# Kernel tuning notes

Hardware: AMD Instinct MI355X
Metric: run time of the kernel (lower is better)

Reference implementation:

```python
import jax, jax.numpy as jnp
import numpy as np

B, S, E = 2, 4096, 640
H, D, G = 4, 256, 1      # n_heads, head_dim, n_kv_groups
WINDOW = 512
SCALING = 256.0 ** -0.5  # query_pre_attn_scalar ** -0.5
EPS = 1e-6


def rmsnorm(x, scale):
    # Gemma variant: weight = 1 + scale, computed in fp32 over last dim
    xf = x.astype(jnp.float32)
    var = jnp.mean(xf * xf, axis=-1, keepdims=True)
    return (xf * jax.lax.rsqrt(var + EPS) * (1.0 + scale.astype(jnp.float32))).astype(x.dtype)


def apply_rope(x, cos, sin):
    # x: [B, h, S, D]; cos/sin: [S, D]
    half = x.shape[-1] // 2
    x1, x2 = x[..., :half], x[..., half:]
    rotated = jnp.concatenate([-x2, x1], axis=-1)
    return (x * cos[None, None] + rotated * sin[None, None]).astype(x.dtype)


def setup_inputs() -> dict:
    key = jax.random.key(0)
    ks = jax.random.split(key, 6)
    x = jax.random.normal(ks[0], (B, S, E), dtype=jnp.float32)
    # weights (torch Linear weight.T layout: [in, out])
    Wq = jax.random.normal(ks[1], (E, H * D), dtype=jnp.float32) * 0.02
    Wk = jax.random.normal(ks[2], (E, G * D), dtype=jnp.float32) * 0.02
    Wv = jax.random.normal(ks[3], (E, G * D), dtype=jnp.float32) * 0.02
    Wo = jax.random.normal(ks[4], (H * D, E), dtype=jnp.float32) * 0.02
    q_scale = jnp.zeros((D,), dtype=jnp.float32)
    k_scale = jnp.zeros((D,), dtype=jnp.float32)
    # RoPE tables (theta = rope_local_base = 10000 for sliding layers)
    inv_freq = 1.0 / (10000.0 ** (jnp.arange(0, D, 2, dtype=jnp.float32) / D))
    angles = jnp.arange(S, dtype=jnp.float32)[:, None] * inv_freq[None, :]
    angles = jnp.concatenate([angles, angles], axis=1)  # [S, D]
    cos, sin = jnp.cos(angles), jnp.sin(angles)
    # causal + sliding-window mask; True = masked out
    i = jnp.arange(S)[:, None]
    j = jnp.arange(S)[None, :]
    mask = (j > i) | ((i - j) >= WINDOW)
    return {"x": x, "mask": mask, "cos": cos, "sin": sin,
            "Wq": Wq, "Wk": Wk, "Wv": Wv, "Wo": Wo,
            "q_scale": q_scale, "k_scale": k_scale}


def reference(x, mask, cos, sin, Wq, Wk, Wv, Wo, q_scale, k_scale):
    b, s, _ = x.shape
    q = (x @ Wq).reshape(b, s, H, D).transpose(0, 2, 1, 3)  # [B,H,S,D]
    k = (x @ Wk).reshape(b, s, G, D).transpose(0, 2, 1, 3)  # [B,G,S,D]
    v = (x @ Wv).reshape(b, s, G, D).transpose(0, 2, 1, 3)  # [B,G,S,D]
    q = rmsnorm(q, q_scale)
    k = rmsnorm(k, k_scale)
    q = apply_rope(q, cos, sin)
    k = apply_rope(k, cos, sin)
    # GQA: K/V have G=1 heads; broadcasting replaces repeat_interleave
    scores = (q * SCALING) @ jnp.swapaxes(k, -1, -2)  # [B,H,S,S]
    scores = jnp.where(mask[None, None], -jnp.inf, scores)
    attn = jax.nn.softmax(scores, axis=-1)
    out = attn @ v                                     # [B,H,S,D]
    out = out.transpose(0, 2, 1, 3).reshape(b, s, H * D)
    return out @ Wo
```

## Files before the change

### kernel.cpp

```cpp
#include <hip/hip_runtime.h>
#include <hip/hip_bf16.h>
#include <stdint.h>

#define BB 2
#define SS 4096
#define EE 640
#define HH 4
#define DD 256
#define WIN 512

typedef __attribute__((ext_vector_type(8))) short bv8;
typedef __attribute__((ext_vector_type(4))) float fv4;
typedef __attribute__((ext_vector_type(16))) float fv16;

__device__ __forceinline__ unsigned short f2b(float f) {
  union { float f; unsigned u; } a; a.f = f;
  unsigned r = a.u + 0x7fffu + ((a.u >> 16) & 1u);
  return (unsigned short)(r >> 16);
}
__device__ __forceinline__ float b2f(unsigned short s) {
  union { unsigned u; float f; } a; a.u = ((unsigned)s) << 16;
  return a.f;
}
__device__ __forceinline__ unsigned pk2(float lo, float hi_) {
  return (unsigned)f2b(lo) | ((unsigned)f2b(hi_) << 16);
}

typedef const __attribute__((address_space(1))) unsigned int* as1u;
typedef __attribute__((address_space(3))) unsigned int* as3u;
__device__ __forceinline__ void gld16(const unsigned short* g, unsigned short* l) {
  __builtin_amdgcn_global_load_lds((as1u)(const void*)g, (as3u)(void*)l, 16, 0, 0);
}

__global__ __launch_bounds__(256) void k_cast_bf16(const float* __restrict__ src,
                                                   unsigned short* __restrict__ dst, int n4) {
  int i = blockIdx.x * 256 + threadIdx.x;
  if (i >= n4) return;
  fv4 v = ((const fv4*)src)[i];
  ushort4 o; o.x = f2b(v.x); o.y = f2b(v.y); o.z = f2b(v.z); o.w = f2b(v.w);
  ((ushort4*)dst)[i] = o;
}

__global__ __launch_bounds__(256) void k_wtrans(const float* __restrict__ Wq,
    const float* __restrict__ Wk, const float* __restrict__ Wv,
    const float* __restrict__ Wo, unsigned short* __restrict__ wqkv,
    unsigned short* __restrict__ wo) {
  __shared__ float tile[32][33];
  const int z = blockIdx.z, bx = blockIdx.x, by = blockIdx.y;
  const float* src; unsigned short* dst; int ss, ds;
  if (z == 0)      { if (bx >= 20 || by >= 32) return; src = Wq; dst = wqkv;              ss = 1024; ds = 640; }
  else if (z == 1) { if (bx >= 20 || by >= 8)  return; src = Wk; dst = wqkv + 1024 * 640; ss = 256;  ds = 640; }
  else if (z == 2) { if (bx >= 20 || by >= 8)  return; src = Wv; dst = wqkv + 1280 * 640; ss = 256;  ds = 640; }
  else             { if (bx >= 32 || by >= 20) return; src = Wo; dst = wo;                ss = 640;  ds = 1024; }
  int r0 = bx * 32, c0 = by * 32;
  int t = threadIdx.x;
  int rr = t >> 3, cc = (t & 7) * 4;
  fv4 x = *(const fv4*)(src + (size_t)(r0 + rr) * ss + c0 + cc);
#pragma unroll
  for (int i = 0; i < 4; ++i) tile[cc + i][rr] = x[i];
  __syncthreads();
  ushort4 o;
  o.x = f2b(tile[rr][cc + 0]); o.y = f2b(tile[rr][cc + 1]);
  o.z = f2b(tile[rr][cc + 2]); o.w = f2b(tile[rr][cc + 3]);
  *(ushort4*)(dst + (size_t)(c0 + rr) * ds + r0 + cc) = o;
}

__global__ __launch_bounds__(256) void k_vtrans(const unsigned short* __restrict__ qkv,
    unsigned short* __restrict__ vt) {
  __shared__ float tile[32][33];
  const int z = blockIdx.z;
  const unsigned short* src = qkv + (size_t)z * 4096 * 1536 + 1280;
  unsigned short* dst = vt + (size_t)z * 256 * 4096;
  int r0 = blockIdx.x * 32, c0 = blockIdx.y * 32;
  int t = threadIdx.x;
  int rr = t >> 3, cc = (t & 7) * 4;
  ushort4 x = *(const ushort4*)(src + (size_t)(r0 + rr) * 1536 + c0 + cc);
  tile[cc + 0][rr] = b2f(x.x); tile[cc + 1][rr] = b2f(x.y);
  tile[cc + 2][rr] = b2f(x.z); tile[cc + 3][rr] = b2f(x.w);
  __syncthreads();
  ushort4 o;
  o.x = f2b(tile[rr][cc + 0]); o.y = f2b(tile[rr][cc + 1]);
  o.z = f2b(tile[rr][cc + 2]); o.w = f2b(tile[rr][cc + 3]);
  *(ushort4*)(dst + (size_t)(c0 + rr) * 4096 + r0 + cc) = o;
}

template <bool OUT_BF16, int BN>
__global__ __launch_bounds__(256) void k_gemm(const unsigned short* __restrict__ A,
    const unsigned short* __restrict__ Bt, void* __restrict__ Cp,
    int M, int N, int K, int nt_n) {
  __shared__ unsigned short la[2][128 * 32];
  __shared__ unsigned short lb[2][BN * 32];
  const int bid = blockIdx.x;
  const int gidx = (bid & 7) * (gridDim.x >> 3) + (bid >> 3);
  const int m0 = (gidx / nt_n) * 128, n0 = (gidx % nt_n) * BN;
  const int tid = threadIdx.x, lane = tid & 63, wave = tid >> 6;
  const int g = lane >> 4, lr = lane & 15;
  constexpr int MI = (BN == 128) ? 4 : 2;
  const int wm = (BN == 128) ? (wave >> 1) * 64 : wave * 32;
  const int wn = (BN == 128) ? (wave & 1) * 64 : 0;
  fv4 acc[MI][4] = {};
  const int srow = wave * 32 + (lane >> 2);
  const int sch = (lane & 3) * 8;
  const unsigned short* ga0 = A + (size_t)(m0 + srow) * K + sch;
  const int srowb = (BN == 128) ? srow : (wave * 16 + (lane >> 2));
  const unsigned short* gb0 = Bt + (size_t)(n0 + srowb) * K + sch;
  const int NIT = K >> 5;
  auto stage = [&](int k0, int pp) {
    unsigned short* lad = la[pp] + wave * 1024;
    unsigned short* lbd = lb[pp] + ((BN == 128) ? wave * 1024 : wave * 512);
    gld16(ga0 + k0, lad);
    gld16(ga0 + (size_t)16 * K + k0, lad + 512);
    gld16(gb0 + k0, lbd);
    if constexpr (BN == 128) gld16(gb0 + (size_t)16 * K + k0, lbd + 512);
  };
  stage(0, 0);
  for (int it = 0; it < NIT; ++it) {
    const int p = it & 1;
    if (it > 0) __builtin_amdgcn_s_barrier();
    if (it + 1 < NIT) {
      stage((it + 1) * 32, p ^ 1);
      if constexpr (BN == 128)
        asm volatile("s_waitcnt vmcnt(4)" ::: "memory");
      else
        asm volatile("s_waitcnt vmcnt(3)" ::: "memory");
    } else {
      asm volatile("s_waitcnt vmcnt(0)" ::: "memory");
    }
    __builtin_amdgcn_sched_barrier(0);
    __builtin_amdgcn_s_barrier();
    bv8 af[MI], bf[4];
#pragma unroll
    for (int mi = 0; mi < MI; ++mi)
      af[mi] = *(const bv8*)(la[p] + (wm + mi * 16 + lr) * 32 + g * 8);
#pragma unroll
    for (int ni = 0; ni < 4; ++ni)
      bf[ni] = *(const bv8*)(lb[p] + (wn + ni * 16 + lr) * 32 + g * 8);
    __builtin_amdgcn_s_setprio(1);
#pragma unroll
    for (int mi = 0; mi < MI; ++mi)
#pragma unroll
      for (int ni = 0; ni < 4; ++ni)
        acc[mi][ni] = __builtin_amdgcn_mfma_f32_16x16x32_bf16(af[mi], bf[ni], acc[mi][ni], 0, 0, 0);
    __builtin_amdgcn_s_setprio(0);
  }
#pragma unroll
  for (int mi = 0; mi < MI; ++mi) {
#pragma unroll
    for (int r = 0; r < 4; ++r) {
      size_t row = (size_t)(m0 + wm + mi * 16 + g * 4 + r);
#pragma unroll
      for (int ni = 0; ni < 4; ++ni) {
        int col = n0 + wn + ni * 16 + lr;
        float val = acc[mi][ni][r];
        if constexpr (OUT_BF16)
          ((unsigned short*)Cp)[row * N + col] = f2b(val);
        else
          ((float*)Cp)[row * N + col] = val;
      }
    }
  }
}

__global__ __launch_bounds__(320) void k_normrope(const unsigned short* __restrict__ qkv,
    const float* __restrict__ cosp, const float* __restrict__ sinp,
    const float* __restrict__ qsc, const float* __restrict__ ksc,
    unsigned short* __restrict__ qo, unsigned short* __restrict__ ko) {
  int m = blockIdx.x;
  int b = m >> 12, s = m & 4095;
  int wave = threadIdx.x >> 6, lane = threadIdx.x & 63;
  bool isq = wave < 4;
  const unsigned short* src = qkv + (size_t)m * 1536 + (isq ? wave * 256 : 1024);
  const float* scp = isq ? qsc : ksc;
  int d0 = lane * 4;
  ushort4 raw = *(const ushort4*)(src + d0);
  float x0 = b2f(raw.x), x1 = b2f(raw.y), x2 = b2f(raw.z), x3 = b2f(raw.w);
  float ss = x0 * x0 + x1 * x1 + x2 * x2 + x3 * x3;
#pragma unroll
  for (int off = 1; off < 64; off <<= 1) ss += __shfl_xor(ss, off, 64);
  float rs = rsqrtf(ss * (1.0f / 256.0f) + 1e-6f);
  fv4 sc = *(const fv4*)(scp + d0);
  float n0 = x0 * rs * (1.0f + sc.x);
  float n1 = x1 * rs * (1.0f + sc.y);
  float n2 = x2 * rs * (1.0f + sc.z);
  float n3 = x3 * rs * (1.0f + sc.w);
  float p0 = __shfl_xor(n0, 32, 64);
  float p1 = __shfl_xor(n1, 32, 64);
  float p2 = __shfl_xor(n2, 32, 64);
  float p3 = __shfl_xor(n3, 32, 64);
  float sgn = (lane < 32) ? -1.0f : 1.0f;
  fv4 c4 = *(const fv4*)(cosp + (size_t)s * 256 + d0);
  fv4 s4 = *(const fv4*)(sinp + (size_t)s * 256 + d0);
  float mult = isq ? (0.0625f * 1.44269504f) : 1.0f;
  float o0 = (n0 * c4.x + sgn * p0 * s4.x) * mult;
  float o1 = (n1 * c4.y + sgn * p1 * s4.y) * mult;
  float o2 = (n2 * c4.z + sgn * p2 * s4.z) * mult;
  float o3 = (n3 * c4.w + sgn * p3 * s4.w) * mult;
  ushort4 o; o.x = f2b(o0); o.y = f2b(o1); o.z = f2b(o2); o.w = f2b(o3);
  unsigned short* dst = isq
      ? qo + ((size_t)(b * HH + wave) * SS + s) * 256 + d0
      : ko + ((size_t)b * SS + s) * 256 + d0;
  *(ushort4*)dst = o;
}

__global__ __launch_bounds__(512, 2) void k_attn(const unsigned short* __restrict__ q,
    const unsigned short* __restrict__ kg, const unsigned short* __restrict__ vtg,
    unsigned short* __restrict__ att) {
  __shared__ __align__(16) char ldsbuf[133120];
  __shared__ float lsb[4][32];
  unsigned short* kt = (unsigned short*)ldsbuf;
  unsigned short* vl = (unsigned short*)ldsbuf + 32768;
  const int bid = blockIdx.x;
  const int gidx = (bid & 7) * 32 + (bid >> 3);
  const int b = gidx >> 7;
  const int i0 = (gidx & 127) * 32;
  const int tid = threadIdx.x, wave = tid >> 6, lane = tid & 63;
  const int h = wave >> 1, ks = wave & 1;
  const int hi = lane >> 5, l31 = lane & 31;
  bv8 qf[16];
  {
    const unsigned short* qp = q + ((size_t)(b * HH + h) * SS + i0 + l31) * 256;
#pragma unroll
    for (int m = 0; m < 16; ++m) qf[m] = *(const bv8*)(qp + m * 16 + hi * 8);
  }
  fv16 po[8] = {};
  float lsp = 0.f;
  const int t0 = (i0 >= WIN) ? ((i0 - WIN + 1) >> 6) : 0;
  const int t1 = i0 >> 6;
  const unsigned short* kb = kg + (size_t)b * SS * 256;
  const unsigned short* vb = vtg + (size_t)b * 256 * SS;
  auto stageK = [&](int t, int pp) {
    const unsigned short* kbase = kb + (size_t)t * 64 * 256;
    unsigned short* dst = kt + pp * 16384;
#pragma unroll
    for (int c = 0; c < 4; ++c) {
      int slot = c * 512 + tid;
      int row = slot >> 5, s = slot & 31;
      gld16(kbase + (size_t)row * 256 + ((s ^ (row & 7)) * 8),
            dst + (c * 512 + wave * 64) * 8);
    }
  };
  auto stageV = [&](int t, int pp) {
    const unsigned short* vbase = vb + (size_t)t * 64;
    unsigned short* dst = vl + pp * 16384;
#pragma unroll
    for (int c = 0; c < 4; ++c) {
      int slot = c * 512 + tid;
      int d_ = slot >> 3, s = slot & 7;
      gld16(vbase + (size_t)d_ * SS + ((s ^ (d_ & 7)) * 8),
            dst + (c * 512 + wave * 64) * 8);
    }
  };
  stageK(t0, 0); stageV(t0, 0);
  int p = 0;
  const int krow = ks * 32 + l31;
  const int krx = krow & 7;
  const int vrx = l31 & 7;
  const float FSUB = 16.5f * 1.44269504f;
  for (int t = t0; t <= t1; ++t) {
    __syncthreads();
    if (t < t1) { stageK(t + 1, p ^ 1); stageV(t + 1, p ^ 1); }
    fv16 sa = {};
    const unsigned short* ktp = kt + p * 16384 + krow * 256;
    __builtin_amdgcn_s_setprio(1);
#pragma unroll
    for (int m = 0; m < 16; ++m) {
      bv8 kf = *(const bv8*)(ktp + (((m * 2 + hi) ^ krx) * 8));
      sa = __builtin_amdgcn_mfma_f32_32x32x16_bf16(kf, qf[m], sa, 0, 0, 0);
    }
    __builtin_amdgcn_s_setprio(0);
    const int kb0 = t * 64 + ks * 32;
    const bool nm = (kb0 + 31 > i0) || (i0 + 31 - kb0 >= WIN);
    if (nm) {
      const int qa = i0 + l31;
#pragma unroll
      for (int r = 0; r < 16; ++r) {
        int j = kb0 + (r & 3) + 8 * (r >> 2) + 4 * hi;
        if (j > qa || qa - j >= WIN) sa[r] = -1e30f;
      }
    }
    unsigned a[8];
#pragma unroll
    for (int i = 0; i < 8; ++i) {
      float e0 = exp2f(sa[2 * i] - FSUB);
      float e1 = exp2f(sa[2 * i + 1] - FSUB);
      lsp += e0 + e1;
      a[i] = pk2(e0, e1);
    }
    const unsigned short* vlp = vl + p * 16384;
    __builtin_amdgcn_s_setprio(1);
#pragma unroll
    for (int m2 = 0; m2 < 2; ++m2) {
      auto r02 = __builtin_amdgcn_permlane32_swap(a[m2 * 4 + 0], a[m2 * 4 + 2], false, false);
      auto r13 = __builtin_amdgcn_permlane32_swap(a[m2 * 4 + 1], a[m2 * 4 + 3], false, false);
      union { unsigned u[4]; bv8 v; } pf;
      pf.u[0] = r02[0]; pf.u[1] = r13[0]; pf.u[2] = r02[1]; pf.u[3] = r13[1];
      const int slot = (ks * 4 + m2 * 2 + hi) ^ vrx;
#pragma unroll
      for (int ds_ = 0; ds_ < 8; ++ds_) {
        bv8 vf = *(const bv8*)(vlp + (ds_ * 32 + l31) * 64 + slot * 8);
        po[ds_] = __builtin_amdgcn_mfma_f32_32x32x16_bf16(vf, pf.v, po[ds_], 0, 0, 0);
      }
    }
    __builtin_amdgcn_s_setprio(0);
    p ^= 1;
  }
  float lsfull = lsp + __shfl_xor(lsp, 32, 64);
  __syncthreads();
  float* cb = (float*)ldsbuf;
  if (ks == 1) {
#pragma unroll
    for (int ds_ = 0; ds_ < 8; ++ds_)
#pragma unroll
      for (int j = 0; j < 4; ++j) {
        int d0 = ds_ * 32 + 8 * j + 4 * hi;
        fv4 v4; v4[0] = po[ds_][4 * j]; v4[1] = po[ds_][4 * j + 1];
        v4[2] = po[ds_][4 * j + 2]; v4[3] = po[ds_][4 * j + 3];
        *(fv4*)(cb + (h * 32 + l31) * 260 + d0) = v4;
      }
    if (lane < 32) lsb[h][lane] = lsfull;
  }
  __syncthreads();
  if (ks == 0) {
    float total = lsfull + lsb[h][l31];
    float inv = 1.0f / total;
    unsigned short* op = att + ((size_t)b * SS + i0 + l31) * 1024 + h * 256;
#pragma unroll
    for (int ds_ = 0; ds_ < 8; ++ds_)
#pragma unroll
      for (int j = 0; j < 4; ++j) {
        int d0 = ds_ * 32 + 8 * j + 4 * hi;
        fv4 v4 = *(const fv4*)(cb + (h * 32 + l31) * 260 + d0);
        ushort4 o;
        o.x = f2b((po[ds_][4 * j] + v4[0]) * inv);
        o.y = f2b((po[ds_][4 * j + 1] + v4[1]) * inv);
        o.z = f2b((po[ds_][4 * j + 2] + v4[2]) * inv);
        o.w = f2b((po[ds_][4 * j + 3] + v4[3]) * inv);
        *(ushort4*)(op + d0) = o;
      }
  }
}

extern "C" void kernel_launch(void* const* d_in, const int* in_sizes, int n_in,
                              void* d_out, int out_size, void* d_ws, size_t ws_size,
                              hipStream_t stream) {
  const float* x    = (const float*)d_in[0];
  const float* cosp = (const float*)d_in[2];
  const float* sinp = (const float*)d_in[3];
  const float* Wq   = (const float*)d_in[4];
  const float* Wk   = (const float*)d_in[5];
  const float* Wv   = (const float*)d_in[6];
  const float* Wo   = (const float*)d_in[7];
  const float* qsc  = (const float*)d_in[8];
  const float* ksc  = (const float*)d_in[9];
  float* out = (float*)d_out;
  char* ws = (char*)d_ws;

  unsigned short* xb   = (unsigned short*)(ws);
  unsigned short* wqkv = (unsigned short*)(ws + 10485760);
  unsigned short* wo   = (unsigned short*)(ws + 12451840);
  unsigned short* qkv  = (unsigned short*)(ws + 13762560);
  unsigned short* qb   = (unsigned short*)(ws + 38928384);
  unsigned short* kbuf = (unsigned short*)(ws + 55705600);
  unsigned short* vt   = (unsigned short*)(ws + 59899904);
  unsigned short* attb = (unsigned short*)(ws + 64094208);

  k_cast_bf16<<<5120, 256, 0, stream>>>(x, xb, 1310720);
  k_wtrans<<<dim3(32, 32, 4), 256, 0, stream>>>(Wq, Wk, Wv, Wo, wqkv, wo);
  k_gemm<true, 128><<<768, 256, 0, stream>>>(xb, wqkv, qkv, 8192, 1536, 640, 12);
  k_normrope<<<8192, 320, 0, stream>>>(qkv, cosp, sinp, qsc, ksc, qb, kbuf);
  k_vtrans<<<dim3(128, 8, 2), 256, 0, stream>>>(qkv, vt);
  k_attn<<<256, 512, 0, stream>>>(qb, kbuf, vt, attb);
  k_gemm<false, 64><<<640, 256, 0, stream>>>(attb, wo, out, 8192, 640, 1024, 10);
}
```

Before: 115.0 us.

## Fuse QKV projection with RMSNorm, RoPE and V transpose epilogue

Replaces the separate QKV GEMM, norm+rope kernel and V-transpose kernel with one GEMM whose tiles are 64x256, so each N-tile covers exactly one head. The epilogue stages the tile in shared memory and applies RMSNorm and RoPE for Q/K heads, or writes V transposed directly. This removes the round trip of the bf16 qkv intermediate through global memory and two kernel launches. In exchange the GEMM tile shape changes (smaller M, larger shared footprint, more registers), which may reduce GEMM efficiency.

```diff
diff --git a/kernel.cpp b/kernel.cpp
--- a/kernel.cpp
+++ b/kernel.cpp
@@ -65,23 +65,142 @@
   *(ushort4*)(dst + (size_t)(c0 + rr) * ds + r0 + cc) = o;
 }
 
-__global__ __launch_bounds__(256) void k_vtrans(const unsigned short* __restrict__ qkv,
+__global__ __launch_bounds__(256) void k_gemm_qkv(const unsigned short* __restrict__ A,
+    const unsigned short* __restrict__ Bt,
+    const float* __restrict__ cosp, const float* __restrict__ sinp,
+    const float* __restrict__ qsc, const float* __restrict__ ksc,
+    unsigned short* __restrict__ qo, unsigned short* __restrict__ ko,
     unsigned short* __restrict__ vt) {
-  __shared__ float tile[32][33];
-  const int z = blockIdx.z;
-  const unsigned short* src = qkv + (size_t)z * 4096 * 1536 + 1280;
-  unsigned short* dst = vt + (size_t)z * 256 * 4096;
-  int r0 = blockIdx.x * 32, c0 = blockIdx.y * 32;
-  int t = threadIdx.x;
-  int rr = t >> 3, cc = (t & 7) * 4;
-  ushort4 x = *(const ushort4*)(src + (size_t)(r0 + rr) * 1536 + c0 + cc);
-  tile[cc + 0][rr] = b2f(x.x); tile[cc + 1][rr] = b2f(x.y);
-  tile[cc + 2][rr] = b2f(x.z); tile[cc + 3][rr] = b2f(x.w);
+  __shared__ __align__(16) char shl[40960];
+  unsigned short* la = (unsigned short*)shl;
+  unsigned short* lb = (unsigned short*)(shl + 8192);
+  const int K = EE;
+  const int bid = blockIdx.x;
+  const int gidx = (bid & 7) * 96 + (bid >> 3);
+  const int mt = gidx / 6, nt = gidx % 6;
+  const int m0 = mt * 64, n0 = nt * 256;
+  const int tid = threadIdx.x, lane = tid & 63, wave = tid >> 6;
+  const int g = lane >> 4, lr = lane & 15;
+  const int wm = (wave >> 1) * 32, wn = (wave & 1) * 128;
+  fv4 acc[2][8] = {};
+  const unsigned short* ga0 = A + (size_t)(m0 + (tid >> 2)) * K + (tid & 3) * 8;
+  const unsigned short* gb0 = Bt + (size_t)(n0 + (tid >> 2)) * K + (tid & 3) * 8;
+  auto stage = [&](int k0, int pp) {
+    gld16(ga0 + k0, la + pp * 2048 + wave * 512);
+#pragma unroll
+    for (int c = 0; c < 4; ++c)
+      gld16(gb0 + (size_t)(c * 64) * K + k0, lb + pp * 8192 + (c * 64 + wave * 16) * 32);
+  };
+  stage(0, 0);
+  const int NIT = K >> 5;
+  for (int it = 0; it < NIT; ++it) {
+    const int p = it & 1;
+    if (it > 0) __builtin_amdgcn_s_barrier();
+    if (it + 1 < NIT) {
+      stage((it + 1) * 32, p ^ 1);
+      asm volatile("s_waitcnt vmcnt(5)" ::: "memory");
+    } else {
+      asm volatile("s_waitcnt vmcnt(0)" ::: "memory");
+    }
+    __builtin_amdgcn_sched_barrier(0);
+    __builtin_amdgcn_s_barrier();
+    bv8 af[2], bf[8];
+#pragma unroll
+    for (int mi = 0; mi < 2; ++mi)
+      af[mi] = *(const bv8*)(la + p * 2048 + (wm + mi * 16 + lr) * 32 + g * 8);
+#pragma unroll
+    for (int ni = 0; ni < 8; ++ni)
+      bf[ni] = *(const bv8*)(lb + p * 8192 + (wn + ni * 16 + lr) * 32 + g * 8);
+    __builtin_amdgcn_s_setprio(1);
+#pragma unroll
+    for (int mi = 0; mi < 2; ++mi)
+#pragma unroll
+      for (int ni = 0; ni < 8; ++ni)
+        acc[mi][ni] = __builtin_amdgcn_mfma_f32_16x16x32_bf16(af[mi], bf[ni], acc[mi][ni], 0, 0, 0);
+    __builtin_amdgcn_s_setprio(0);
+  }
   __syncthreads();
-  ushort4 o;
-  o.x = f2b(tile[rr][cc + 0]); o.y = f2b(tile[rr][cc + 1]);
-  o.z = f2b(tile[rr][cc + 2]); o.w = f2b(tile[rr][cc + 3]);
-  *(ushort4*)(dst + (size_t)(c0 + rr) * 4096 + r0 + cc) = o;
+  unsigned short* cw = (unsigned short*)shl;
+  float* rsum = (float*)(shl + 33792);
+#pragma unroll
+  for (int mi = 0; mi < 2; ++mi)
+#pragma unroll
+    for (int r = 0; r < 4; ++r) {
+      int row = wm + mi * 16 + g * 4 + r;
+#pragma unroll
+      for (int ni = 0; ni < 8; ++ni)
+        cw[row * 264 + wn + ni * 16 + lr] = f2b(acc[mi][ni][r]);
+    }
+  __syncthreads();
+  const int m = m0 + (tid & 63);
+  const int b = m >> 12, s = m & 4095;
+  if (nt < 5) {
+    const int qq = tid >> 6;
+    const int row = tid & 63;
+    const int dlo = qq * 32, dhi = dlo + 128;
+    float xlo[32], xhi[32];
+    float ss2 = 0.f;
+#pragma unroll
+    for (int j8 = 0; j8 < 4; ++j8) {
+      bv8 v0 = *(const bv8*)(cw + row * 264 + dlo + j8 * 8);
+      bv8 v1 = *(const bv8*)(cw + row * 264 + dhi + j8 * 8);
+#pragma unroll
+      for (int e = 0; e < 8; ++e) {
+        float a0 = b2f((unsigned short)v0[e]);
+        float a1 = b2f((unsigned short)v1[e]);
+        xlo[j8 * 8 + e] = a0; xhi[j8 * 8 + e] = a1;
+        ss2 += a0 * a0 + a1 * a1;
+      }
+    }
+    rsum[row * 4 + qq] = ss2;
+    __syncthreads();
+    float tot = rsum[row * 4 + 0] + rsum[row * 4 + 1] + rsum[row * 4 + 2] + rsum[row * 4 + 3];
+    float rs = rsqrtf(tot * (1.0f / 256.0f) + 1e-6f);
+    const float* scp = (nt < 4) ? qsc : ksc;
+    const float mult = (nt < 4) ? (0.0625f * 1.44269504f) : 1.0f;
+    unsigned short* dst = (nt < 4)
+        ? qo + ((size_t)(b * HH + nt) * SS + s) * 256
+        : ko + ((size_t)b * SS + s) * 256;
+    const float* crow = cosp + (size_t)s * 256;
+    const float* srow = sinp + (size_t)s * 256;
+#pragma unroll
+    for (int j4 = 0; j4 < 8; ++j4) {
+      fv4 sclo = *(const fv4*)(scp + dlo + j4 * 4);
+      fv4 schi = *(const fv4*)(scp + dhi + j4 * 4);
+      fv4 clo = *(const fv4*)(crow + dlo + j4 * 4);
+      fv4 chi = *(const fv4*)(crow + dhi + j4 * 4);
+      fv4 slo = *(const fv4*)(srow + dlo + j4 * 4);
+      fv4 shi = *(const fv4*)(srow + dhi + j4 * 4);
+      ushort4 olo, ohi;
+#pragma unroll
+      for (int e = 0; e < 4; ++e) {
+        float nlo = xlo[j4 * 4 + e] * rs * (1.0f + sclo[e]);
+        float nhi = xhi[j4 * 4 + e] * rs * (1.0f + schi[e]);
+        float rlo = (nlo * clo[e] - nhi * slo[e]) * mult;
+        float rhi = (nhi * chi[e] + nlo * shi[e]) * mult;
+        ((unsigned short*)&olo)[e] = f2b(rlo);
+        ((unsigned short*)&ohi)[e] = f2b(rhi);
+      }
+      *(ushort4*)(dst + dlo + j4 * 4) = olo;
+      *(ushort4*)(dst + dhi + j4 * 4) = ohi;
+    }
+  } else {
+    const int d = tid;
+    const int bb2 = (m0 >> 12), s0 = m0 & 4095;
+    ushort4 buf[16];
+#pragma unroll
+    for (int r4 = 0; r4 < 16; ++r4) {
+      ushort4 o;
+      o.x = cw[(r4 * 4 + 0) * 264 + d];
+      o.y = cw[(r4 * 4 + 1) * 264 + d];
+      o.z = cw[(r4 * 4 + 2) * 264 + d];
+      o.w = cw[(r4 * 4 + 3) * 264 + d];
+      buf[r4] = o;
+    }
+    unsigned short* dst = vt + ((size_t)bb2 * 256 + d) * SS + s0;
+#pragma unroll
+    for (int r4 = 0; r4 < 16; ++r4) *(ushort4*)(dst + r4 * 4) = buf[r4];
+  }
 }
 
 template <bool OUT_BF16, int BN>
@@ -161,47 +280,6 @@
   }
 }
 
-__global__ __launch_bounds__(320) void k_normrope(const unsigned short* __restrict__ qkv,
-    const float* __restrict__ cosp, const float* __restrict__ sinp,
-    const float* __restrict__ qsc, const float* __restrict__ ksc,
-    unsigned short* __restrict__ qo, unsigned short* __restrict__ ko) {
-  int m = blockIdx.x;
-  int b = m >> 12, s = m & 4095;
-  int wave = threadIdx.x >> 6, lane = threadIdx.x & 63;
-  bool isq = wave < 4;
-  const unsigned short* src = qkv + (size_t)m * 1536 + (isq ? wave * 256 : 1024);
-  const float* scp = isq ? qsc : ksc;
-  int d0 = lane * 4;
-  ushort4 raw = *(const ushort4*)(src + d0);
-  float x0 = b2f(raw.x), x1 = b2f(raw.y), x2 = b2f(raw.z), x3 = b2f(raw.w);
-  float ss = x0 * x0 + x1 * x1 + x2 * x2 + x3 * x3;
-#pragma unroll
-  for (int off = 1; off < 64; off <<= 1) ss += __shfl_xor(ss, off, 64);
-  float rs = rsqrtf(ss * (1.0f / 256.0f) + 1e-6f);
-  fv4 sc = *(const fv4*)(scp + d0);
-  float n0 = x0 * rs * (1.0f + sc.x);
-  float n1 = x1 * rs * (1.0f + sc.y);
-  float n2 = x2 * rs * (1.0f + sc.z);
-  float n3 = x3 * rs * (1.0f + sc.w);
-  float p0 = __shfl_xor(n0, 32, 64);
-  float p1 = __shfl_xor(n1, 32, 64);
-  float p2 = __shfl_xor(n2, 32, 64);
-  float p3 = __shfl_xor(n3, 32, 64);
-  float sgn = (lane < 32) ? -1.0f : 1.0f;
-  fv4 c4 = *(const fv4*)(cosp + (size_t)s * 256 + d0);
-  fv4 s4 = *(const fv4*)(sinp + (size_t)s * 256 + d0);
-  float mult = isq ? (0.0625f * 1.44269504f) : 1.0f;
-  float o0 = (n0 * c4.x + sgn * p0 * s4.x) * mult;
-  float o1 = (n1 * c4.y + sgn * p1 * s4.y) * mult;
-  float o2 = (n2 * c4.z + sgn * p2 * s4.z) * mult;
-  float o3 = (n3 * c4.w + sgn * p3 * s4.w) * mult;
-  ushort4 o; o.x = f2b(o0); o.y = f2b(o1); o.z = f2b(o2); o.w = f2b(o3);
-  unsigned short* dst = isq
-      ? qo + ((size_t)(b * HH + wave) * SS + s) * 256 + d0
-      : ko + ((size_t)b * SS + s) * 256 + d0;
-  *(ushort4*)dst = o;
-}
-
 __global__ __launch_bounds__(512, 2) void k_attn(const unsigned short* __restrict__ q,
     const unsigned short* __restrict__ kg, const unsigned short* __restrict__ vtg,
     unsigned short* __restrict__ att) {
@@ -358,7 +436,6 @@
   unsigned short* xb   = (unsigned short*)(ws);
   unsigned short* wqkv = (unsigned short*)(ws + 10485760);
   unsigned short* wo   = (unsigned short*)(ws + 12451840);
-  unsigned short* qkv  = (unsigned short*)(ws + 13762560);
   unsigned short* qb   = (unsigned short*)(ws + 38928384);
   unsigned short* kbuf = (unsigned short*)(ws + 55705600);
   unsigned short* vt   = (unsigned short*)(ws + 59899904);
@@ -366,9 +443,7 @@
 
   k_cast_bf16<<<5120, 256, 0, stream>>>(x, xb, 1310720);
   k_wtrans<<<dim3(32, 32, 4), 256, 0, stream>>>(Wq, Wk, Wv, Wo, wqkv, wo);
-  k_gemm<true, 128><<<768, 256, 0, stream>>>(xb, wqkv, qkv, 8192, 1536, 640, 12);
-  k_normrope<<<8192, 320, 0, stream>>>(qkv, cosp, sinp, qsc, ksc, qb, kbuf);
-  k_vtrans<<<dim3(128, 8, 2), 256, 0, stream>>>(qkv, vt);
+  k_gemm_qkv<<<768, 256, 0, stream>>>(xb, wqkv, cosp, sinp, qsc, ksc, qb, kbuf, vt);
   k_attn<<<256, 512, 0, stream>>>(qb, kbuf, vt, attb);
   k_gemm<false, 64><<<640, 256, 0, stream>>>(attb, wo, out, 8192, 640, 1024, 10);
 }
```

After: 126.9 us. 10.3% more time.
